# Performance work log

Hardware: AMD Instinct MI355X
Metric: run time of the kernel (lower is better)

Reference implementation:

```python
import jax, jax.numpy as jnp
import numpy as np

D_MODEL = 768
N_HEADS = 12
HEAD_DIM = D_MODEL // N_HEADS


def rotary_emb(seq_len, dim):
    # matches RotaryEmbedding: emb = concat(sin(freqs), cos(freqs)) over last dim
    inv_freq = 1.0 / (10000.0 ** (jnp.arange(0, dim, 2, dtype=jnp.float32) / dim))
    t = jnp.arange(seq_len, dtype=jnp.float32)
    freqs = t[:, None] * inv_freq[None, :]            # [T, dim/2]
    return jnp.concatenate([jnp.sin(freqs), jnp.cos(freqs)], axis=-1)  # [T, dim]


def apply_rotary_pos_emb(x, emb):
    # faithful to the source's (quirky) interleaved slicing of the concat'd emb
    x1, x2 = x[..., ::2], x[..., 1::2]
    sin, cos = emb[..., ::2], emb[..., 1::2]
    return jnp.concatenate([x1 * cos - x2 * sin, x1 * sin + x2 * cos], axis=-1)


def setup_inputs() -> dict:
    key = jax.random.key(0)
    ks = jax.random.split(key, 14)
    B, Tq, Tk = 2, 2048, 4096
    s = 1.0 / np.sqrt(D_MODEL)
    return {
        "query": jax.random.normal(ks[0], (B, Tq, D_MODEL), jnp.float32),
        "key": jax.random.normal(ks[1], (B, Tk, D_MODEL), jnp.float32),
        "value": jax.random.normal(ks[2], (B, Tk, D_MODEL), jnp.float32),
        "Wq": jax.random.normal(ks[3], (D_MODEL, D_MODEL), jnp.float32) * s,
        "bq": jnp.zeros((D_MODEL,), jnp.float32),
        "Wk": jax.random.normal(ks[4], (D_MODEL, D_MODEL), jnp.float32) * s,
        "bk": jnp.zeros((D_MODEL,), jnp.float32),
        "Wv": jax.random.normal(ks[5], (D_MODEL, D_MODEL), jnp.float32) * s,
        "bv": jnp.zeros((D_MODEL,), jnp.float32),
        "Wo": jax.random.normal(ks[6], (D_MODEL, D_MODEL), jnp.float32) * s,
        "bo": jnp.zeros((D_MODEL,), jnp.float32),
    }


def reference(query, key, value, Wq, bq, Wk, bk, Wv, bv, Wo, bo):
    B, Tq, _ = query.shape
    Tk = key.shape[1]
    H, D = N_HEADS, HEAD_DIM

    q = (query @ Wq.T + bq).reshape(B, Tq, H, D).transpose(0, 2, 1, 3)  # [B,H,Tq,D]
    k = (key @ Wk.T + bk).reshape(B, Tk, H, D).transpose(0, 2, 1, 3)    # [B,H,Tk,D]
    v = (value @ Wv.T + bv).reshape(B, Tk, H, D).transpose(0, 2, 1, 3)  # [B,H,Tk,D]

    q = apply_rotary_pos_emb(q, rotary_emb(Tq, D)[None, None, :, :])
    k = apply_rotary_pos_emb(k, rotary_emb(Tk, D)[None, None, :, :])

    scores = jnp.einsum("bhqd,bhkd->bhqk", q, k) / jnp.sqrt(jnp.float32(D))
    weights = jax.nn.softmax(scores, axis=-1)
    attn = jnp.einsum("bhqk,bhkd->bhqd", weights, v)  # [B,H,Tq,D]

    out = attn.transpose(0, 2, 1, 3).reshape(B, Tq, H * D)
    return out @ Wo.T + bo
```

## Files before the change

### kernel.cpp

```cpp
#include <hip/hip_runtime.h>
#include <hip/hip_bf16.h>
#include <math.h>

#define DM 768
#define HEADS 12
#define BQ 2
#define TQ 2048
#define TK 4096
#define NSPLIT 4
#define KTS (TK / 64 / NSPLIT)
#define ROWS (BQ * HEADS * TQ)

typedef __attribute__((ext_vector_type(8))) short bf16x8;
typedef __attribute__((ext_vector_type(4))) float f32x4;
typedef __attribute__((ext_vector_type(16))) float f32x16;
typedef __attribute__((ext_vector_type(4))) short short4v;
typedef __attribute__((ext_vector_type(2))) unsigned uint2v;

__device__ inline unsigned pk2bf(float a, float b) {
    union { __hip_bfloat162 h; unsigned u; } c;
    c.h = __float22bfloat162_rn(make_float2(a, b));
    return c.u;
}
__device__ inline short f2bf(float f) { return (short)(pk2bf(f, f) & 0xffffu); }

__device__ inline float bf2f(short s) {
    union { unsigned u; float f; } a; a.u = ((unsigned)(unsigned short)s) << 16;
    return a.f;
}

__device__ inline void plswap(unsigned &a, unsigned &b) {
    uint2v r = __builtin_amdgcn_permlane32_swap(a, b, false, false);
    a = r[0]; b = r[1];
}
__device__ inline void plswap2(unsigned &a, unsigned &b, unsigned x) {
    uint2v r = __builtin_amdgcn_permlane32_swap(x, x, false, false);
    a = r[0]; b = r[1];
}

__global__ void rope_tables(float2* scu) {
    int idx = blockIdx.x * 256 + threadIdx.x;
    if (idx >= TK * 32) return;
    int t = idx >> 5, j = idx & 31;
    double su, cu;
    if (j < 16) {
        su = sin((double)t * pow(10000.0, -(double)(2 * (2 * j)) / 64.0));
        cu = sin((double)t * pow(10000.0, -(double)(2 * (2 * j + 1)) / 64.0));
    } else {
        su = cos((double)t * pow(10000.0, -(double)(2 * (2 * j - 32)) / 64.0));
        cu = cos((double)t * pow(10000.0, -(double)(2 * (2 * j - 31)) / 64.0));
    }
    scu[idx] = make_float2((float)su, (float)cu);
}

__global__ __launch_bounds__(256) void gemm_qkv(
        const float* __restrict__ query, const float* __restrict__ key_,
        const float* __restrict__ value,
        const float* __restrict__ Wq, const float* __restrict__ bq,
        const float* __restrict__ Wk, const float* __restrict__ bk,
        const float* __restrict__ Wv, const float* __restrict__ bv,
        const float2* __restrict__ scu,
        short* __restrict__ qh, short* __restrict__ kh, short* __restrict__ vt,
        float qscale) {
    __shared__ short Alds[64 * 72];
    __shared__ short Blds[128 * 72];
    const int tid = threadIdx.x;
    const int lane = tid & 63, wid = tid >> 6;
    const int wr = wid >> 1, wc = wid & 1;
    const int l4 = lane >> 4, l15 = lane & 15;
    const int id = blockIdx.x;
    const int xcd = id & 7, pos = id >> 3;
    const int bx = xcd * 40 + pos / 6;
    const int bn = (pos % 6) * 128;

    const float* X; const float* W; const float* bias;
    short* dst; int bm, tsh, mode; float scale;
    if (bx < 64)       { X = query; W = Wq; bias = bq; dst = qh; bm = bx * 64;         tsh = 11; mode = 0; scale = qscale; }
    else if (bx < 192) { X = key_;  W = Wk; bias = bk; dst = kh; bm = (bx - 64) * 64;  tsh = 12; mode = 0; scale = 1.f; }
    else               { X = value; W = Wv; bias = bv; dst = vt; bm = (bx - 192) * 64; tsh = 12; mode = 1; scale = 1.f; }
    const int T = 1 << tsh, tmask = T - 1;

    int srA[4], skA[4], srB[8], skB[8];
#pragma unroll
    for (int p = 0; p < 4; ++p) {
        int c = p * 256 + tid;
        srA[p] = c >> 4; skA[p] = (c & 15) * 4;
    }
#pragma unroll
    for (int p = 0; p < 8; ++p) {
        int c = p * 256 + tid;
        srB[p] = c >> 4; skB[p] = (c & 15) * 4;
    }
    const float* Xb = X + (size_t)bm * DM;
    const float* Wb = W + (size_t)bn * DM;

    f32x4 acc[2][4] = {};
    float4 fa[4], fw[8];

#pragma unroll
    for (int p = 0; p < 4; ++p)
        fa[p] = *reinterpret_cast<const float4*>(&Xb[(size_t)srA[p] * DM + skA[p]]);
#pragma unroll
    for (int p = 0; p < 8; ++p)
        fw[p] = *reinterpret_cast<const float4*>(&Wb[(size_t)srB[p] * DM + skB[p]]);

    for (int k0 = 0; k0 < DM; k0 += 64) {
#pragma unroll
        for (int p = 0; p < 4; ++p) {
            uint2v s; s.x = pk2bf(fa[p].x, fa[p].y); s.y = pk2bf(fa[p].z, fa[p].w);
            *reinterpret_cast<uint2v*>(&Alds[srA[p] * 72 + skA[p]]) = s;
        }
#pragma unroll
        for (int p = 0; p < 8; ++p) {
            uint2v t4; t4.x = pk2bf(fw[p].x, fw[p].y); t4.y = pk2bf(fw[p].z, fw[p].w);
            *reinterpret_cast<uint2v*>(&Blds[srB[p] * 72 + skB[p]]) = t4;
        }
        __syncthreads();

        if (k0 + 64 < DM) {
#pragma unroll
            for (int p = 0; p < 4; ++p)
                fa[p] = *reinterpret_cast<const float4*>(&Xb[(size_t)srA[p] * DM + k0 + 64 + skA[p]]);
#pragma unroll
            for (int p = 0; p < 8; ++p)
                fw[p] = *reinterpret_cast<const float4*>(&Wb[(size_t)srB[p] * DM + k0 + 64 + skB[p]]);
        }

#pragma unroll
        for (int kk = 0; kk < 2; ++kk) {
            bf16x8 af[2], bfr[4];
#pragma unroll
            for (int i = 0; i < 2; ++i)
                af[i] = *reinterpret_cast<const bf16x8*>(&Alds[(wr * 32 + i * 16 + l15) * 72 + kk * 32 + l4 * 8]);
#pragma unroll
            for (int j = 0; j < 4; ++j)
                bfr[j] = *reinterpret_cast<const bf16x8*>(&Blds[(wc * 64 + j * 16 + l15) * 72 + kk * 32 + l4 * 8]);
            __builtin_amdgcn_s_setprio(1);
#pragma unroll
            for (int i = 0; i < 2; ++i)
#pragma unroll
                for (int j = 0; j < 4; ++j)
                    acc[i][j] = __builtin_amdgcn_mfma_f32_16x16x32_bf16(af[i], bfr[j], acc[i][j], 0, 0, 0);
            __builtin_amdgcn_s_setprio(0);
        }
        __syncthreads();
    }

    if (mode == 0) {
#pragma unroll
        for (int i = 0; i < 2; ++i) {
            int mrow0 = bm + wr * 32 + i * 16 + l4 * 4;
#pragma unroll
            for (int j = 0; j < 4; ++j) {
                int n = bn + wc * 64 + j * 16 + l15;
                int hh = n >> 6, c = n & 63, u = c >> 1, odd = c & 1;
                float bb = bias[n];
#pragma unroll
                for (int r = 0; r < 4; ++r) {
                    float val = acc[i][j][r] + bb;
                    float pv = __shfl_xor(val, 1);
                    int mrow = mrow0 + r;
                    int b_ = mrow >> tsh, t = mrow & tmask;
                    float2 sc = scu[t * 32 + u];
                    float outv = odd ? (pv * sc.x + val * sc.y)
                                     : (val * sc.y - pv * sc.x);
                    int d = (odd << 5) + u;
                    dst[((size_t)(b_ * HEADS + hh) * T + t) * 64 + d] = f2bf(outv * scale);
                }
            }
        }
    } else {
#pragma unroll
        for (int i = 0; i < 2; ++i) {
            int mrow0 = bm + wr * 32 + i * 16 + l4 * 4;
            int b_ = mrow0 >> 12, t = mrow0 & 4095;
#pragma unroll
            for (int j = 0; j < 4; ++j) {
                int n = bn + wc * 64 + j * 16 + l15;
                int hh = n >> 6, dd = n & 63;
                float bb = bias[n];
                uint2v s;
                s.x = pk2bf(acc[i][j][0] + bb, acc[i][j][1] + bb);
                s.y = pk2bf(acc[i][j][2] + bb, acc[i][j][3] + bb);
                *reinterpret_cast<uint2v*>(
                    &dst[((size_t)(b_ * HEADS + hh) * 64 + dd) * TK + t]) = s;
            }
        }
    }
}

__global__ __launch_bounds__(256) void gemm_out(const short* __restrict__ Xh,
                                                const float* __restrict__ W,
                                                const float* __restrict__ bias,
                                                float* __restrict__ Y) {
    __shared__ short Alds[128 * 40];
    __shared__ short Blds[128 * 40];
    const int tid = threadIdx.x;
    const int lane = tid & 63, wid = tid >> 6;
    const int wr = wid >> 1, wc = wid & 1;
    const int l4 = lane >> 4, l15 = lane & 15;
    const int id = blockIdx.x;
    const int xcd = id & 7, pos = id >> 3;
    const int bm = (xcd * 4 + pos / 6) * 128;
    const int bn = (pos % 6) * 128;

    int srow[4], skq[4];
#pragma unroll
    for (int p = 0; p < 4; ++p) {
        int c = p * 256 + tid;
        srow[p] = c >> 3; skq[p] = (c & 7) * 4;
    }

    f32x4 acc[4][4] = {};
    short4v ra[4]; float4 fw[4];

#pragma unroll
    for (int p = 0; p < 4; ++p) {
        ra[p] = *reinterpret_cast<const short4v*>(&Xh[(size_t)(bm + srow[p]) * DM + skq[p]]);
        fw[p] = *reinterpret_cast<const float4*>(&W[(size_t)(bn + srow[p]) * DM + skq[p]]);
    }

    for (int k0 = 0; k0 < DM; k0 += 32) {
#pragma unroll
        for (int p = 0; p < 4; ++p) {
            *reinterpret_cast<short4v*>(&Alds[srow[p] * 40 + skq[p]]) = ra[p];
            uint2v t4; t4.x = pk2bf(fw[p].x, fw[p].y); t4.y = pk2bf(fw[p].z, fw[p].w);
            *reinterpret_cast<uint2v*>(&Blds[srow[p] * 40 + skq[p]]) = t4;
        }
        __syncthreads();

        if (k0 + 32 < DM) {
#pragma unroll
            for (int p = 0; p < 4; ++p) {
                ra[p] = *reinterpret_cast<const short4v*>(&Xh[(size_t)(bm + srow[p]) * DM + k0 + 32 + skq[p]]);
                fw[p] = *reinterpret_cast<const float4*>(&W[(size_t)(bn + srow[p]) * DM + k0 + 32 + skq[p]]);
            }
        }

        bf16x8 af[4], bfr[4];
#pragma unroll
        for (int i = 0; i < 4; ++i)
            af[i] = *reinterpret_cast<const bf16x8*>(&Alds[(wr * 64 + i * 16 + l15) * 40 + l4 * 8]);
#pragma unroll
        for (int j = 0; j < 4; ++j)
            bfr[j] = *reinterpret_cast<const bf16x8*>(&Blds[(wc * 64 + j * 16 + l15) * 40 + l4 * 8]);
        __builtin_amdgcn_s_setprio(1);
#pragma unroll
        for (int i = 0; i < 4; ++i)
#pragma unroll
            for (int j = 0; j < 4; ++j)
                acc[i][j] = __builtin_amdgcn_mfma_f32_16x16x32_bf16(af[i], bfr[j], acc[i][j], 0, 0, 0);
        __builtin_amdgcn_s_setprio(0);
        __syncthreads();
    }

#pragma unroll
    for (int i = 0; i < 4; ++i) {
        int m = bm + wr * 64 + i * 16 + l4 * 4;
#pragma unroll
        for (int j = 0; j < 4; ++j) {
            int n = bn + wc * 64 + j * 16 + l15;
            float bb = bias[n];
#pragma unroll
            for (int r = 0; r < 4; ++r)
                Y[(size_t)(m + r) * DM + n] = acc[i][j][r] + bb;
        }
    }
}

__global__ __launch_bounds__(256, 4) void attn(const short* __restrict__ qh,
                                               const short* __restrict__ kh,
                                               const short* __restrict__ vt,
                                               short* __restrict__ Opart,
                                               float* __restrict__ ml) {
    __shared__ short Ks[2][64 * 64];
    __shared__ short Vs[2][64 * 64];
    const int id = blockIdx.x;
    const int hs = id % 96, qt = id / 96;
    const int h = hs % HEADS, rest = hs / HEADS;
    const int split = rest & 3, b = rest >> 2;
    const int tid = threadIdx.x, lane = tid & 63, w = tid >> 6;
    const int l31 = lane & 31, hi = lane >> 5;
    const size_t bh = (size_t)(b * HEADS + h);
    const short* kbase = kh + bh * TK * 64;
    const short* vbase = vt + bh * (size_t)64 * TK;
    const int t0 = split * KTS;

#define SWZ(row, bo) ((row) * 64 + ((((bo)) ^ (((row) & 7) << 4)) >> 1))
#define KGLB(c, t_) (kbase + ((size_t)(t_) * 64 + ((c) >> 3)) * 64 + ((c) & 7) * 8)
#define VGLB(c, t_) (vbase + (size_t)((c) >> 3) * TK + (t_) * 64 + ((c) & 7) * 8)

    int loff[2][4];
#pragma unroll
    for (int t2 = 0; t2 < 2; ++t2)
#pragma unroll
        for (int d0 = 0; d0 < 4; ++d0)
            loff[t2][d0] = SWZ(t2 * 32 + l31, d0 * 32 + hi * 16);

    bf16x8 qf[4];
    {
        const short* qrow = qh + (bh * TQ + (size_t)qt * 128 + w * 32 + l31) * 64 + hi * 8;
#pragma unroll
        for (int d0 = 0; d0 < 4; ++d0)
            qf[d0] = *reinterpret_cast<const bf16x8*>(qrow + d0 * 16);
    }

    f32x16 oacc[2] = {};
    float lsum = 0.f;

    const int c0 = tid, c1 = tid + 256;
    const int sw0 = SWZ(c0 >> 3, (c0 & 7) * 16), sw1 = SWZ(c1 >> 3, (c1 & 7) * 16);

    {
        bf16x8 k0 = *reinterpret_cast<const bf16x8*>(KGLB(c0, t0));
        bf16x8 k1 = *reinterpret_cast<const bf16x8*>(KGLB(c1, t0));
        bf16x8 v0 = *reinterpret_cast<const bf16x8*>(VGLB(c0, t0));
        bf16x8 v1 = *reinterpret_cast<const bf16x8*>(VGLB(c1, t0));
        *reinterpret_cast<bf16x8*>(&Ks[0][sw0]) = k0;
        *reinterpret_cast<bf16x8*>(&Ks[0][sw1]) = k1;
        *reinterpret_cast<bf16x8*>(&Vs[0][sw0]) = v0;
        *reinterpret_cast<bf16x8*>(&Vs[0][sw1]) = v1;
    }
    __syncthreads();

    int cur = 0;
    for (int kt = 0; kt < KTS; ++kt) {
        const bool pre = (kt + 1 < KTS);
        bf16x8 sk0, sk1, sv0, sv1;
        if (pre) {
            sk0 = *reinterpret_cast<const bf16x8*>(KGLB(c0, t0 + kt + 1));
            sk1 = *reinterpret_cast<const bf16x8*>(KGLB(c1, t0 + kt + 1));
            sv0 = *reinterpret_cast<const bf16x8*>(VGLB(c0, t0 + kt + 1));
            sv1 = *reinterpret_cast<const bf16x8*>(VGLB(c1, t0 + kt + 1));
        }

        f32x16 sacc[2] = {};
        __builtin_amdgcn_s_setprio(1);
#pragma unroll
        for (int t2 = 0; t2 < 2; ++t2)
#pragma unroll
            for (int d0 = 0; d0 < 4; ++d0) {
                bf16x8 kf = *reinterpret_cast<const bf16x8*>(&Ks[cur][loff[t2][d0]]);
                sacc[t2] = __builtin_amdgcn_mfma_f32_32x32x16_bf16(kf, qf[d0], sacc[t2], 0, 0, 0);
            }
        __builtin_amdgcn_s_setprio(0);

#pragma unroll
        for (int t2 = 0; t2 < 2; ++t2)
#pragma unroll
            for (int i = 0; i < 16; ++i)
                sacc[t2][i] = exp2f(sacc[t2][i]);
        float s8[8];
#pragma unroll
        for (int i = 0; i < 8; ++i)
            s8[i] = (sacc[0][i] + sacc[0][i + 8]) + (sacc[1][i] + sacc[1][i + 8]);
        float rs = ((s8[0] + s8[1]) + (s8[2] + s8[3])) + ((s8[4] + s8[5]) + (s8[6] + s8[7]));
        {
            unsigned a, bb2;
            plswap2(a, bb2, __float_as_uint(rs));
            rs = __uint_as_float(a) + __uint_as_float(bb2);
        }
        lsum += rs;

#define PP(idx) (sacc[(idx) >> 4][(idx) & 15])
        bf16x8 pa[4];
#pragma unroll
        for (int ks = 0; ks < 4; ++ks) {
            const int base = (ks >> 1) * 16 + (ks & 1) * 8;
            unsigned u0 = pk2bf(PP(base + 0), PP(base + 1));
            unsigned u1 = pk2bf(PP(base + 2), PP(base + 3));
            unsigned u2 = pk2bf(PP(base + 4), PP(base + 5));
            unsigned u3 = pk2bf(PP(base + 6), PP(base + 7));
            plswap(u0, u2);
            plswap(u1, u3);
            union { unsigned u[4]; bf16x8 v; } asm_;
            asm_.u[0] = u0; asm_.u[1] = u1; asm_.u[2] = u2; asm_.u[3] = u3;
            pa[ks] = asm_.v;
        }
#undef PP

        if (pre) {
            *reinterpret_cast<bf16x8*>(&Ks[cur ^ 1][sw0]) = sk0;
            *reinterpret_cast<bf16x8*>(&Ks[cur ^ 1][sw1]) = sk1;
            *reinterpret_cast<bf16x8*>(&Vs[cur ^ 1][sw0]) = sv0;
            *reinterpret_cast<bf16x8*>(&Vs[cur ^ 1][sw1]) = sv1;
        }

        __builtin_amdgcn_s_setprio(1);
#pragma unroll
        for (int dt = 0; dt < 2; ++dt)
#pragma unroll
            for (int ks = 0; ks < 4; ++ks) {
                bf16x8 vf = *reinterpret_cast<const bf16x8*>(&Vs[cur][loff[dt][ks]]);
                oacc[dt] = __builtin_amdgcn_mfma_f32_32x32x16_bf16(vf, pa[ks], oacc[dt], 0, 0, 0);
            }
        __builtin_amdgcn_s_setprio(0);

        __syncthreads();
        cur ^= 1;
    }

    float rln = 1.f / lsum;
    const size_t R = bh * TQ + (size_t)qt * 128 + w * 32 + l31;
    const size_t obase = ((size_t)split * ROWS + R) * 64;
#pragma unroll
    for (int dt = 0; dt < 2; ++dt)
#pragma unroll
        for (int rq = 0; rq < 4; ++rq) {
            uint2v st;
            st.x = pk2bf(oacc[dt][rq * 4 + 0] * rln, oacc[dt][rq * 4 + 1] * rln);
            st.y = pk2bf(oacc[dt][rq * 4 + 2] * rln, oacc[dt][rq * 4 + 3] * rln);
            *reinterpret_cast<uint2v*>(&Opart[obase + dt * 32 + rq * 8 + hi * 4]) = st;
        }
    if (hi == 0)
        ml[(size_t)split * ROWS + R] = lsum;
#undef SWZ
#undef KGLB
#undef VGLB
}

__global__ __launch_bounds__(256) void attn_combine(const short* __restrict__ Opart,
                                                    const float* __restrict__ ml,
                                                    short* __restrict__ attnO) {
    int idx = blockIdx.x * 256 + threadIdx.x;
    int R = idx >> 3, g = idx & 7;
    float wgt[NSPLIT], L = 0.f;
#pragma unroll
    for (int s = 0; s < NSPLIT; ++s) {
        wgt[s] = ml[(size_t)s * ROWS + R];
        L += wgt[s];
    }
    float rL = 1.f / L;
    float o[8] = {};
#pragma unroll
    for (int s = 0; s < NSPLIT; ++s) {
        float c = wgt[s] * rL;
        bf16x8 v = *reinterpret_cast<const bf16x8*>(&Opart[(((size_t)s * ROWS + R) * 64) + g * 8]);
#pragma unroll
        for (int i = 0; i < 8; ++i) o[i] += c * bf2f(v[i]);
    }
    int bh = R >> 11, t = R & 2047;
    int b = bh / HEADS, h = bh - b * HEADS;
    uint2v s0, s1;
    s0.x = pk2bf(o[0], o[1]); s0.y = pk2bf(o[2], o[3]);
    s1.x = pk2bf(o[4], o[5]); s1.y = pk2bf(o[6], o[7]);
    size_t dst = (((size_t)b * TQ + t) * HEADS + h) * 64 + g * 8;
    *reinterpret_cast<uint2v*>(&attnO[dst]) = s0;
    *reinterpret_cast<uint2v*>(&attnO[dst + 4]) = s1;
}

extern "C" void kernel_launch(void* const* d_in, const int* in_sizes, int n_in,
                              void* d_out, int out_size, void* d_ws, size_t ws_size,
                              hipStream_t stream) {
    const float* query = (const float*)d_in[0];
    const float* key_  = (const float*)d_in[1];
    const float* value = (const float*)d_in[2];
    const float* Wq = (const float*)d_in[3];
    const float* bq = (const float*)d_in[4];
    const float* Wk = (const float*)d_in[5];
    const float* bk = (const float*)d_in[6];
    const float* Wv = (const float*)d_in[7];
    const float* bv = (const float*)d_in[8];
    const float* Wo = (const float*)d_in[9];
    const float* bo = (const float*)d_in[10];
    float* out = (float*)d_out;

    char* ws = (char*)d_ws;
    float2* scu  = (float2*)(ws + 0);
    short* qh    = (short*)(ws + 1048576);
    short* kh    = (short*)(ws + 7340032);
    short* vt    = (short*)(ws + 19922944);
    short* attnO = (short*)(ws + 32505856);
    short* Opart = (short*)(ws + 38797312);
    float* ml    = (float*)(ws + 63963136);

    dim3 blk(256);
    const float QSCALE = 0.125f * 1.44269504088896341f;

    rope_tables<<<(TK * 32 + 255) / 256, blk, 0, stream>>>(scu);
    gemm_qkv<<<dim3(1920), blk, 0, stream>>>(query, key_, value, Wq, bq, Wk, bk,
                                             Wv, bv, scu, qh, kh, vt, QSCALE);
    attn<<<dim3(16 * 96), blk, 0, stream>>>(qh, kh, vt, Opart, ml);
    attn_combine<<<ROWS * 8 / 256, blk, 0, stream>>>(Opart, ml, attnO);
    gemm_out<<<dim3(192), blk, 0, stream>>>(attnO, Wo, bo, out);
}
```

Before: 190.2 us.

## Stream QKV GEMM activations into LDS with direct global-to-LDS loads

The A-operand (activation) tile of the QKV projection GEMM is now copied straight from global memory into a double-buffered fp32 LDS tile with global_load_lds. It uses an XOR-swizzled layout, and the bf16 conversion moves to the point where MFMA fragments are read. This removes the register staging and the separate convert-and-store step for A, and lets the next tile's load overlap the current tile's compute. In exchange it uses more LDS (fp32 and two buffers), which can lower occupancy, and repeats the conversion work across the waves that read each fragment.

Result: slower. 199.6 us (+4.9%).

```diff
diff --git a/kernel.cpp b/kernel.cpp
--- a/kernel.cpp
+++ b/kernel.cpp
@@ -36,6 +36,12 @@
 __device__ inline void plswap2(unsigned &a, unsigned &b, unsigned x) {
     uint2v r = __builtin_amdgcn_permlane32_swap(x, x, false, false);
     a = r[0]; b = r[1];
+}
+
+__device__ inline void glds16(const void* g, void* l) {
+    __builtin_amdgcn_global_load_lds(
+        (const __attribute__((address_space(1))) unsigned*)g,
+        (__attribute__((address_space(3))) unsigned*)l, 16, 0, 0);
 }
 
 __global__ void rope_tables(float2* scu) {
@@ -62,7 +68,7 @@
         const float2* __restrict__ scu,
         short* __restrict__ qh, short* __restrict__ kh, short* __restrict__ vt,
         float qscale) {
-    __shared__ short Alds[64 * 72];
+    __shared__ float Af[2][64 * 64];
     __shared__ short Blds[128 * 72];
     const int tid = threadIdx.x;
     const int lane = tid & 63, wid = tid >> 6;
@@ -80,36 +86,45 @@
     else               { X = value; W = Wv; bias = bv; dst = vt; bm = (bx - 192) * 64; tsh = 12; mode = 1; scale = 1.f; }
     const int T = 1 << tsh, tmask = T - 1;
 
-    int srA[4], skA[4], srB[8], skB[8];
-#pragma unroll
-    for (int p = 0; p < 4; ++p) {
-        int c = p * 256 + tid;
-        srA[p] = c >> 4; skA[p] = (c & 15) * 4;
-    }
+    const float* Xb = X + (size_t)bm * DM;
+    const float* Wb = W + (size_t)bn * DM;
+
+    const char* XbB = (const char*)Xb;
+    size_t srcA[4];
+#pragma unroll
+    for (int q = 0; q < 4; ++q) {
+        int off16 = (wid * 4 + q) * 64 + lane;
+        int r = off16 >> 4, u = off16 & 15;
+        int g2 = u >> 1, h = u & 1;
+        srcA[q] = (size_t)r * DM * 4 + (size_t)(((g2 ^ (r & 7)) << 5) + (h << 4));
+    }
+    const int rg = l15 & 7;
+    int aoff[2][2];
+#pragma unroll
+    for (int i = 0; i < 2; ++i)
+#pragma unroll
+        for (int kk = 0; kk < 2; ++kk)
+            aoff[i][kk] = (wr * 32 + i * 16 + l15) * 64 + (((kk * 4 + l4) ^ rg) << 3);
+
+    int srB[8], skB[8];
 #pragma unroll
     for (int p = 0; p < 8; ++p) {
         int c = p * 256 + tid;
         srB[p] = c >> 4; skB[p] = (c & 15) * 4;
     }
-    const float* Xb = X + (size_t)bm * DM;
-    const float* Wb = W + (size_t)bn * DM;
 
     f32x4 acc[2][4] = {};
-    float4 fa[4], fw[8];
-
-#pragma unroll
-    for (int p = 0; p < 4; ++p)
-        fa[p] = *reinterpret_cast<const float4*>(&Xb[(size_t)srA[p] * DM + skA[p]]);
+    float4 fw[8];
+
+#pragma unroll
+    for (int q = 0; q < 4; ++q)
+        glds16(XbB + srcA[q], &Af[0][(wid * 4 + q) * 256]);
 #pragma unroll
     for (int p = 0; p < 8; ++p)
         fw[p] = *reinterpret_cast<const float4*>(&Wb[(size_t)srB[p] * DM + skB[p]]);
 
+    int cur = 0;
     for (int k0 = 0; k0 < DM; k0 += 64) {
-#pragma unroll
-        for (int p = 0; p < 4; ++p) {
-            uint2v s; s.x = pk2bf(fa[p].x, fa[p].y); s.y = pk2bf(fa[p].z, fa[p].w);
-            *reinterpret_cast<uint2v*>(&Alds[srA[p] * 72 + skA[p]]) = s;
-        }
 #pragma unroll
         for (int p = 0; p < 8; ++p) {
             uint2v t4; t4.x = pk2bf(fw[p].x, fw[p].y); t4.y = pk2bf(fw[p].z, fw[p].w);
@@ -119,8 +134,9 @@
 
         if (k0 + 64 < DM) {
 #pragma unroll
-            for (int p = 0; p < 4; ++p)
-                fa[p] = *reinterpret_cast<const float4*>(&Xb[(size_t)srA[p] * DM + k0 + 64 + skA[p]]);
+            for (int q = 0; q < 4; ++q)
+                glds16(XbB + (size_t)(k0 + 64) * 4 + srcA[q],
+                       &Af[cur ^ 1][(wid * 4 + q) * 256]);
 #pragma unroll
             for (int p = 0; p < 8; ++p)
                 fw[p] = *reinterpret_cast<const float4*>(&Wb[(size_t)srB[p] * DM + k0 + 64 + skB[p]]);
@@ -130,8 +146,15 @@
         for (int kk = 0; kk < 2; ++kk) {
             bf16x8 af[2], bfr[4];
 #pragma unroll
-            for (int i = 0; i < 2; ++i)
-                af[i] = *reinterpret_cast<const bf16x8*>(&Alds[(wr * 32 + i * 16 + l15) * 72 + kk * 32 + l4 * 8]);
+            for (int i = 0; i < 2; ++i) {
+                const float* ap = &Af[cur][aoff[i][kk]];
+                float4 x0 = *reinterpret_cast<const float4*>(ap);
+                float4 x1 = *reinterpret_cast<const float4*>(ap + 4);
+                union { unsigned u[4]; bf16x8 v; } cc;
+                cc.u[0] = pk2bf(x0.x, x0.y); cc.u[1] = pk2bf(x0.z, x0.w);
+                cc.u[2] = pk2bf(x1.x, x1.y); cc.u[3] = pk2bf(x1.z, x1.w);
+                af[i] = cc.v;
+            }
 #pragma unroll
             for (int j = 0; j < 4; ++j)
                 bfr[j] = *reinterpret_cast<const bf16x8*>(&Blds[(wc * 64 + j * 16 + l15) * 72 + kk * 32 + l4 * 8]);
@@ -144,6 +167,7 @@
             __builtin_amdgcn_s_setprio(0);
         }
         __syncthreads();
+        cur ^= 1;
     }
 
     if (mode == 0) {
```
